# Kernel tuning notes

Hardware: AMD Instinct MI355X
Metric: run time of the kernel (lower is better)

Reference implementation:

```python
import jax, jax.numpy as jnp
import numpy as np

B, D, H, W = 16, 128, 64, 64
K = 512  # num_embeddings


def setup_inputs() -> dict:
    key = jax.random.key(0)
    k1, k2 = jax.random.split(key)
    inputs = jax.random.normal(k1, (B, D, H, W), dtype=jnp.float32)
    embedding_weight = jax.random.normal(k2, (K, D), dtype=jnp.float32)
    return {"inputs": inputs, "embedding_weight": embedding_weight}


def reference(inputs, embedding_weight):
    # NCHW -> NHWC, flatten to [N, D]
    x = jnp.transpose(inputs, (0, 2, 3, 1))  # [B, H, W, D]
    flat = x.reshape(-1, x.shape[-1])        # [N, D]
    dists = (
        jnp.sum(flat ** 2, axis=1, keepdims=True)
        + jnp.sum(embedding_weight ** 2, axis=1)
        - 2.0 * flat @ embedding_weight.T
    )  # [N, K]
    idx = jnp.argmin(dists, axis=1)          # [N]
    # one-hot @ codebook == gather
    quantized = embedding_weight[idx].reshape(x.shape)  # [B, H, W, D]
    # straight-through estimator
    quantized = x + jax.lax.stop_gradient(quantized - x)
    return jnp.transpose(quantized, (0, 3, 1, 2))  # back to NCHW
```

## Files before the change

### kernel.cpp

```cpp
#include <hip/hip_runtime.h>


typedef _Float16 f16;
typedef _Float16 f16x4 __attribute__((ext_vector_type(4)));
typedef _Float16 f16x8 __attribute__((ext_vector_type(8)));
typedef float f32x16 __attribute__((ext_vector_type(16)));

#define ND 128
#define NK 512
#define NHW 4096
#define LO_SCALE 2048.0f
#define LO_INV (1.0f / 2048.0f)

#define WS_EHI 0
#define WS_ELO 131072u
#define WS_ENS 262144u
#define WS_NEED 264192u

__global__ __launch_bounds__(256) void vq_prep_e(const float* __restrict__ e,
                                                 f16* __restrict__ ehi, f16* __restrict__ elo,
                                                 float* __restrict__ ens) {
  const int tid = threadIdx.x;
  const int k0 = (int)blockIdx.x * 16;
  const int r = tid >> 4, dq16 = tid & 15;
  const int k = k0 + r;
  float ssum = 0.0f;
  #pragma unroll
  for (int hh = 0; hh < 2; ++hh) {
    const int dq = dq16 + 16 * hh;
    const float4 v = *(const float4*)(e + (size_t)k * ND + 4 * dq);
    ssum += v.x * v.x + v.y * v.y + v.z * v.z + v.w * v.w;
    float va[4] = {v.x, v.y, v.z, v.w};
    f16x4 hv, lv;
    #pragma unroll
    for (int j = 0; j < 4; ++j) {
      const f16 h = (f16)va[j];
      hv[j] = h;
      lv[j] = (f16)((va[j] - (float)h) * LO_SCALE);
    }
    const int sl = (dq >> 1) ^ (k & 15);
    const size_t off = (size_t)k * ND + sl * 8 + (dq & 1) * 4;
    *(f16x4*)(ehi + off) = hv;
    *(f16x4*)(elo + off) = lv;
  }
  #pragma unroll
  for (int m = 1; m < 16; m <<= 1) ssum += __shfl_xor(ssum, m, 64);
  if (dq16 == 0) ens[k] = 0.5f * ssum;
}

__global__ __launch_bounds__(256) void vq_score(const float* __restrict__ x,
                                                const f16* __restrict__ ehi,
                                                const f16* __restrict__ elo,
                                                const float* __restrict__ ens,
                                                const float* __restrict__ e32,
                                                float* __restrict__ out) {
  __shared__ f16 eh_s[2][64 * 128];
  __shared__ f16 el_s[2][64 * 128];
  __shared__ float ens_s[NK];

  const int tid = threadIdx.x;
  const int w = tid >> 6;
  const int lane = tid & 63;
  const int l31 = lane & 31;
  const int half = lane >> 5;
  const int T0 = (int)blockIdx.x * 128;
  const int tok = T0 + w * 32 + l31;
  const int bb = tok >> 12;
  const int hw = tok & 4095;

  #pragma unroll
  for (int p = 0; p < 4; ++p) {
    __builtin_amdgcn_global_load_lds(ehi + p * 2048 + tid * 8, &eh_s[0][p * 2048 + tid * 8], 16, 0, 0);
    __builtin_amdgcn_global_load_lds(elo + p * 2048 + tid * 8, &el_s[0][p * 2048 + tid * 8], 16, 0, 0);
  }

  f16x8 Bh[8], Bl[8];
  {
    const float* xb = x + (size_t)bb * ND * NHW + hw;
    #pragma unroll
    for (int ks = 0; ks < 8; ++ks) {
      const int oct = 2 * ks + half;
      #pragma unroll
      for (int j = 0; j < 8; ++j) {
        const float v = xb[(size_t)(oct * 8 + j) * NHW];
        const f16 hv = (f16)v;
        Bh[ks][j] = hv;
        Bl[ks][j] = (f16)((v - (float)hv) * LO_SCALE);
      }
    }
  }
  ens_s[tid] = ens[tid];
  ens_s[tid + 256] = ens[tid + 256];
  __syncthreads();

  float bv = -3.0e38f;
  int bi = 0;
  const int sbase = l31 & 15;

  for (int c = 0; c < 8; ++c) {
    const int cur = c & 1;
    if (c < 7) {
      const f16* gh = ehi + (c + 1) * 8192;
      const f16* gl = elo + (c + 1) * 8192;
      f16* dh = &eh_s[cur ^ 1][0];
      f16* dl = &el_s[cur ^ 1][0];
      #pragma unroll
      for (int p = 0; p < 4; ++p) {
        __builtin_amdgcn_global_load_lds(gh + p * 2048 + tid * 8, dh + p * 2048 + tid * 8, 16, 0, 0);
        __builtin_amdgcn_global_load_lds(gl + p * 2048 + tid * 8, dl + p * 2048 + tid * 8, 16, 0, 0);
      }
    }
    #pragma unroll
    for (int cg = 0; cg < 2; ++cg) {
      const int r = cg * 32 + l31;
      const f16* ah = &eh_s[cur][r * 128];
      const f16* al = &el_s[cur][r * 128];
      f32x16 a1 = {}, a2 = {};
      __builtin_amdgcn_s_setprio(1);
      #pragma unroll
      for (int ks = 0; ks < 8; ++ks) {
        const int sl = ((2 * ks + half) ^ sbase) * 8;
        const f16x8 Ah = *(const f16x8*)(ah + sl);
        const f16x8 Al = *(const f16x8*)(al + sl);
        a2 = __builtin_amdgcn_mfma_f32_32x32x16_f16(Al, Bh[ks], a2, 0, 0, 0);
        a1 = __builtin_amdgcn_mfma_f32_32x32x16_f16(Ah, Bh[ks], a1, 0, 0, 0);
        a2 = __builtin_amdgcn_mfma_f32_32x32x16_f16(Ah, Bl[ks], a2, 0, 0, 0);
      }
      __builtin_amdgcn_s_setprio(0);
      const int kb = c * 64 + cg * 32 + 4 * half;
      const float4 b0 = *(const float4*)&ens_s[kb + 0];
      const float4 b1 = *(const float4*)&ens_s[kb + 8];
      const float4 b2 = *(const float4*)&ens_s[kb + 16];
      const float4 b3 = *(const float4*)&ens_s[kb + 24];
      const float bias[16] = {b0.x, b0.y, b0.z, b0.w, b1.x, b1.y, b1.z, b1.w,
                              b2.x, b2.y, b2.z, b2.w, b3.x, b3.y, b3.z, b3.w};
      #pragma unroll
      for (int rr = 0; rr < 16; ++rr) {
        const float s = a1[rr] + a2[rr] * LO_INV - bias[rr];
        const int code = kb + (rr & 3) + 8 * (rr >> 2);
        if (s > bv) { bv = s; bi = code; }
      }
    }
    __syncthreads();
  }

  {
    const float ov = __shfl_xor(bv, 32, 64);
    const int oi = __shfl_xor(bi, 32, 64);
    if (ov > bv || (ov == bv && oi < bi)) { bv = ov; bi = oi; }
  }

  {
    const float* er = e32 + (size_t)bi * ND + half * 64;
    float* ob = out + (size_t)bb * ND * NHW + (size_t)(half * 64) * NHW + hw;
    #pragma unroll
    for (int j4 = 0; j4 < 16; ++j4) {
      const float4 ev = *(const float4*)(er + j4 * 4);
      ob[(size_t)(j4 * 4 + 0) * NHW] = ev.x;
      ob[(size_t)(j4 * 4 + 1) * NHW] = ev.y;
      ob[(size_t)(j4 * 4 + 2) * NHW] = ev.z;
      ob[(size_t)(j4 * 4 + 3) * NHW] = ev.w;
    }
  }
}

__global__ __launch_bounds__(128) void vq_enorm(const float* __restrict__ e,
                                                float* __restrict__ ensw) {
  const int k = blockIdx.x;
  const int d = threadIdx.x;
  const float v = e[k * ND + d];
  float s = v * v;
  #pragma unroll
  for (int off = 32; off > 0; off >>= 1) s += __shfl_down(s, off, 64);
  __shared__ float tmp[2];
  if ((d & 63) == 0) tmp[d >> 6] = s;
  __syncthreads();
  if (d == 0) ensw[k] = tmp[0] + tmp[1];
}

__global__ __launch_bounds__(256, 2) void vq_main_f32(const float* __restrict__ x,
                                                      const float* __restrict__ e,
                                                      const float* __restrict__ ensw,
                                                      float* __restrict__ out) {
  __shared__ float xs[ND][64];
  __shared__ float esh[ND][64];
  __shared__ float enh[NK];
  __shared__ float red_v[64][17];
  __shared__ int red_i[64][17];
  __shared__ int bidx[64];
  const int tid = threadIdx.x;
  const int b = blockIdx.x >> 6;
  const int hw0 = (blockIdx.x & 63) * 64;
  const float* xb = x + ((size_t)b * ND) * NHW;
  #pragma unroll
  for (int i = 0; i < 8; ++i) {
    const int f = tid + 256 * i;
    const int d = f >> 4, t4 = f & 15;
    const float4 v = *(const float4*)(xb + (size_t)d * NHW + hw0 + 4 * t4);
    *(float4*)&xs[d][4 * t4] = v;
  }
  #pragma unroll
  for (int i = 0; i < 2; ++i) enh[tid + 256 * i] = ensw[tid + 256 * i];
  const int t4 = tid & 15, m = tid >> 4;
  float bvv[4] = {-3.0e38f, -3.0e38f, -3.0e38f, -3.0e38f};
  int bii[4] = {0, 0, 0, 0};
  for (int kc = 0; kc < NK / 64; ++kc) {
    __syncthreads();
    #pragma unroll
    for (int i = 0; i < 8; ++i) {
      const int f = tid + 256 * i;
      const int kk = f & 63, dq = f >> 6;
      const float4 v = *(const float4*)(e + (size_t)(kc * 64 + kk) * ND + 4 * dq);
      esh[4 * dq + 0][kk] = v.x; esh[4 * dq + 1][kk] = v.y;
      esh[4 * dq + 2][kk] = v.z; esh[4 * dq + 3][kk] = v.w;
    }
    __syncthreads();
    float acc[4][4];
    #pragma unroll
    for (int a = 0; a < 4; ++a)
      #pragma unroll
      for (int cc = 0; cc < 4; ++cc) acc[a][cc] = 0.0f;
    #pragma unroll 8
    for (int d = 0; d < ND; ++d) {
      const float4 xv = *(const float4*)&xs[d][4 * t4];
      const float4 ev = *(const float4*)&esh[d][4 * m];
      const float xa[4] = {xv.x, xv.y, xv.z, xv.w};
      const float ea[4] = {ev.x, ev.y, ev.z, ev.w};
      #pragma unroll
      for (int a = 0; a < 4; ++a)
        #pragma unroll
        for (int cc = 0; cc < 4; ++cc) acc[a][cc] = fmaf(xa[a], ea[cc], acc[a][cc]);
    }
    const int kbase = kc * 64 + 4 * m;
    #pragma unroll
    for (int cc = 0; cc < 4; ++cc) {
      const float bias = 0.5f * enh[kbase + cc];
      const int kg = kbase + cc;
      #pragma unroll
      for (int a = 0; a < 4; ++a) {
        const float s = acc[a][cc] - bias;
        if (s > bvv[a] || (s == bvv[a] && kg < bii[a])) { bvv[a] = s; bii[a] = kg; }
      }
    }
  }
  #pragma unroll
  for (int a = 0; a < 4; ++a) { red_v[4 * t4 + a][m] = bvv[a]; red_i[4 * t4 + a][m] = bii[a]; }
  __syncthreads();
  if (tid < 64) {
    float v = red_v[tid][0]; int ix = red_i[tid][0];
    #pragma unroll
    for (int j = 1; j < 16; ++j) {
      const float vj = red_v[tid][j]; const int ij = red_i[tid][j];
      if (vj > v || (vj == v && ij < ix)) { v = vj; ix = ij; }
    }
    bidx[tid] = ix;
  }
  __syncthreads();
  const int t = tid & 63, dgg = tid >> 6;
  const float* er = e + (size_t)bidx[t] * ND;
  float* ob = out + ((size_t)b * ND) * NHW + hw0 + t;
  #pragma unroll
  for (int i = 0; i < 32; ++i) ob[(size_t)(dgg * 32 + i) * NHW] = er[dgg * 32 + i];
}

extern "C" void kernel_launch(void* const* d_in, const int* in_sizes, int n_in,
                              void* d_out, int out_size, void* d_ws, size_t ws_size,
                              hipStream_t stream) {
  const float* x = (const float*)d_in[0];
  const float* e = (const float*)d_in[1];
  float* out = (float*)d_out;
  char* ws = (char*)d_ws;

  if (ws_size >= WS_NEED) {
    f16* ehi = (f16*)(ws + WS_EHI);
    f16* elo = (f16*)(ws + WS_ELO);
    float* ens = (float*)(ws + WS_ENS);
    vq_prep_e<<<32, 256, 0, stream>>>(e, ehi, elo, ens);
    vq_score<<<512, 256, 0, stream>>>(x, ehi, elo, ens, e, out);
  } else {
    float* ensw = (float*)d_ws;
    vq_enorm<<<NK, 128, 0, stream>>>(e, ensw);
    vq_main_f32<<<16 * 64, 256, 0, stream>>>(x, e, ensw, out);
  }
}
```

Before: 45.76 us.

## Process two token tiles per wave to reuse codebook LDS reads

Each wave now handles 64 tokens as two 32-token MFMA tiles, so every codebook fragment read from LDS feeds twice as many MFMAs. The grid is halved to 256 blocks, launch bounds are set to one block per SIMD group, and the s_setprio hints are dropped. This cuts LDS traffic and codebook global reloads per token. In exchange it raises register pressure, since B fragments and accumulators double, and with 256 CUs the grid now covers only one wave of blocks, which lowers latency hiding.

```diff
diff --git a/kernel.cpp b/kernel.cpp
--- a/kernel.cpp
+++ b/kernel.cpp
@@ -48,12 +48,12 @@
   if (dq16 == 0) ens[k] = 0.5f * ssum;
 }
 
-__global__ __launch_bounds__(256) void vq_score(const float* __restrict__ x,
-                                                const f16* __restrict__ ehi,
-                                                const f16* __restrict__ elo,
-                                                const float* __restrict__ ens,
-                                                const float* __restrict__ e32,
-                                                float* __restrict__ out) {
+__global__ __launch_bounds__(256, 1) void vq_score(const float* __restrict__ x,
+                                                   const f16* __restrict__ ehi,
+                                                   const f16* __restrict__ elo,
+                                                   const float* __restrict__ ens,
+                                                   const float* __restrict__ e32,
+                                                   float* __restrict__ out) {
   __shared__ f16 eh_s[2][64 * 128];
   __shared__ f16 el_s[2][64 * 128];
   __shared__ float ens_s[NK];
@@ -63,10 +63,13 @@
   const int lane = tid & 63;
   const int l31 = lane & 31;
   const int half = lane >> 5;
-  const int T0 = (int)blockIdx.x * 128;
-  const int tok = T0 + w * 32 + l31;
-  const int bb = tok >> 12;
-  const int hw = tok & 4095;
+  const int T0 = (int)blockIdx.x * 256;
+  const int tok0 = T0 + w * 64 + l31;
+  const int tok1 = tok0 + 32;
+  const int bb = T0 >> 12;
+  const int hw0 = tok0 & 4095;
+  const int hw1 = tok1 & 4095;
+  const int sbase = l31 & 15;
 
   #pragma unroll
   for (int p = 0; p < 4; ++p) {
@@ -74,18 +77,23 @@
     __builtin_amdgcn_global_load_lds(elo + p * 2048 + tid * 8, &el_s[0][p * 2048 + tid * 8], 16, 0, 0);
   }
 
-  f16x8 Bh[8], Bl[8];
+  f16x8 B0h[8], B0l[8], B1h[8], B1l[8];
   {
-    const float* xb = x + (size_t)bb * ND * NHW + hw;
+    const float* xb0 = x + (size_t)bb * ND * NHW + hw0;
+    const float* xb1 = x + (size_t)bb * ND * NHW + hw1;
     #pragma unroll
     for (int ks = 0; ks < 8; ++ks) {
       const int oct = 2 * ks + half;
       #pragma unroll
       for (int j = 0; j < 8; ++j) {
-        const float v = xb[(size_t)(oct * 8 + j) * NHW];
-        const f16 hv = (f16)v;
-        Bh[ks][j] = hv;
-        Bl[ks][j] = (f16)((v - (float)hv) * LO_SCALE);
+        const float v0 = xb0[(size_t)(oct * 8 + j) * NHW];
+        const float v1 = xb1[(size_t)(oct * 8 + j) * NHW];
+        const f16 h0 = (f16)v0;
+        const f16 h1 = (f16)v1;
+        B0h[ks][j] = h0;
+        B0l[ks][j] = (f16)((v0 - (float)h0) * LO_SCALE);
+        B1h[ks][j] = h1;
+        B1l[ks][j] = (f16)((v1 - (float)h1) * LO_SCALE);
       }
     }
   }
@@ -93,9 +101,8 @@
   ens_s[tid + 256] = ens[tid + 256];
   __syncthreads();
 
-  float bv = -3.0e38f;
-  int bi = 0;
-  const int sbase = l31 & 15;
+  float bv0 = -3.0e38f, bv1 = -3.0e38f;
+  int bi0 = 0, bi1 = 0;
 
   for (int c = 0; c < 8; ++c) {
     const int cur = c & 1;
@@ -115,18 +122,19 @@
       const int r = cg * 32 + l31;
       const f16* ah = &eh_s[cur][r * 128];
       const f16* al = &el_s[cur][r * 128];
-      f32x16 a1 = {}, a2 = {};
-      __builtin_amdgcn_s_setprio(1);
+      f32x16 a1_0 = {}, a2_0 = {}, a1_1 = {}, a2_1 = {};
       #pragma unroll
       for (int ks = 0; ks < 8; ++ks) {
         const int sl = ((2 * ks + half) ^ sbase) * 8;
         const f16x8 Ah = *(const f16x8*)(ah + sl);
         const f16x8 Al = *(const f16x8*)(al + sl);
-        a2 = __builtin_amdgcn_mfma_f32_32x32x16_f16(Al, Bh[ks], a2, 0, 0, 0);
-        a1 = __builtin_amdgcn_mfma_f32_32x32x16_f16(Ah, Bh[ks], a1, 0, 0, 0);
-        a2 = __builtin_amdgcn_mfma_f32_32x32x16_f16(Ah, Bl[ks], a2, 0, 0, 0);
-      }
-      __builtin_amdgcn_s_setprio(0);
+        a2_0 = __builtin_amdgcn_mfma_f32_32x32x16_f16(Al, B0h[ks], a2_0, 0, 0, 0);
+        a2_1 = __builtin_amdgcn_mfma_f32_32x32x16_f16(Al, B1h[ks], a2_1, 0, 0, 0);
+        a1_0 = __builtin_amdgcn_mfma_f32_32x32x16_f16(Ah, B0h[ks], a1_0, 0, 0, 0);
+        a1_1 = __builtin_amdgcn_mfma_f32_32x32x16_f16(Ah, B1h[ks], a1_1, 0, 0, 0);
+        a2_0 = __builtin_amdgcn_mfma_f32_32x32x16_f16(Ah, B0l[ks], a2_0, 0, 0, 0);
+        a2_1 = __builtin_amdgcn_mfma_f32_32x32x16_f16(Ah, B1l[ks], a2_1, 0, 0, 0);
+      }
       const int kb = c * 64 + cg * 32 + 4 * half;
       const float4 b0 = *(const float4*)&ens_s[kb + 0];
       const float4 b1 = *(const float4*)&ens_s[kb + 8];
@@ -136,30 +144,42 @@
                               b2.x, b2.y, b2.z, b2.w, b3.x, b3.y, b3.z, b3.w};
       #pragma unroll
       for (int rr = 0; rr < 16; ++rr) {
-        const float s = a1[rr] + a2[rr] * LO_INV - bias[rr];
         const int code = kb + (rr & 3) + 8 * (rr >> 2);
-        if (s > bv) { bv = s; bi = code; }
+        const float s0 = a1_0[rr] + a2_0[rr] * LO_INV - bias[rr];
+        const float s1 = a1_1[rr] + a2_1[rr] * LO_INV - bias[rr];
+        if (s0 > bv0) { bv0 = s0; bi0 = code; }
+        if (s1 > bv1) { bv1 = s1; bi1 = code; }
       }
     }
     __syncthreads();
   }
 
   {
-    const float ov = __shfl_xor(bv, 32, 64);
-    const int oi = __shfl_xor(bi, 32, 64);
-    if (ov > bv || (ov == bv && oi < bi)) { bv = ov; bi = oi; }
+    const float o0 = __shfl_xor(bv0, 32, 64);
+    const int i0 = __shfl_xor(bi0, 32, 64);
+    if (o0 > bv0 || (o0 == bv0 && i0 < bi0)) { bv0 = o0; bi0 = i0; }
+    const float o1 = __shfl_xor(bv1, 32, 64);
+    const int i1 = __shfl_xor(bi1, 32, 64);
+    if (o1 > bv1 || (o1 == bv1 && i1 < bi1)) { bv1 = o1; bi1 = i1; }
   }
 
   {
-    const float* er = e32 + (size_t)bi * ND + half * 64;
-    float* ob = out + (size_t)bb * ND * NHW + (size_t)(half * 64) * NHW + hw;
+    const float* er0 = e32 + (size_t)bi0 * ND + half * 64;
+    const float* er1 = e32 + (size_t)bi1 * ND + half * 64;
+    float* ob0 = out + (size_t)bb * ND * NHW + (size_t)(half * 64) * NHW + hw0;
+    float* ob1 = out + (size_t)bb * ND * NHW + (size_t)(half * 64) * NHW + hw1;
     #pragma unroll
     for (int j4 = 0; j4 < 16; ++j4) {
-      const float4 ev = *(const float4*)(er + j4 * 4);
-      ob[(size_t)(j4 * 4 + 0) * NHW] = ev.x;
-      ob[(size_t)(j4 * 4 + 1) * NHW] = ev.y;
-      ob[(size_t)(j4 * 4 + 2) * NHW] = ev.z;
-      ob[(size_t)(j4 * 4 + 3) * NHW] = ev.w;
+      const float4 e0 = *(const float4*)(er0 + j4 * 4);
+      const float4 e1 = *(const float4*)(er1 + j4 * 4);
+      ob0[(size_t)(j4 * 4 + 0) * NHW] = e0.x;
+      ob0[(size_t)(j4 * 4 + 1) * NHW] = e0.y;
+      ob0[(size_t)(j4 * 4 + 2) * NHW] = e0.z;
+      ob0[(size_t)(j4 * 4 + 3) * NHW] = e0.w;
+      ob1[(size_t)(j4 * 4 + 0) * NHW] = e1.x;
+      ob1[(size_t)(j4 * 4 + 1) * NHW] = e1.y;
+      ob1[(size_t)(j4 * 4 + 2) * NHW] = e1.z;
+      ob1[(size_t)(j4 * 4 + 3) * NHW] = e1.w;
     }
   }
 }
@@ -276,7 +296,7 @@
     f16* elo = (f16*)(ws + WS_ELO);
     float* ens = (float*)(ws + WS_ENS);
     vq_prep_e<<<32, 256, 0, stream>>>(e, ehi, elo, ens);
-    vq_score<<<512, 256, 0, stream>>>(x, ehi, elo, ens, e, out);
+    vq_score<<<256, 256, 0, stream>>>(x, ehi, elo, ens, e, out);
   } else {
     float* ensw = (float*)d_ws;
     vq_enorm<<<NK, 128, 0, stream>>>(e, ensw);
```

Result: slower. 53.24 us (+16.3%).
